# Optimization experiments

Measured on AMD Instinct MI355X. Metric: run time of the kernel, lower is better.

## Reference

```python
import jax, jax.numpy as jnp
import numpy as np

B, T, I, H = 64, 128, 1024, 4096
NNZ_IH, NNZ_HH = 262144, 1048576
LN_EPS = 1e-5


def spmm(rows, cols, vals, x, n_out):
    # y[r, b] = sum_{e: rows[e]==r} vals[e] * x[cols[e], b]
    return jax.ops.segment_sum(vals[:, None] * x[cols], rows, num_segments=n_out)


def setup_inputs() -> dict:
    key = jax.random.key(0)
    ks = jax.random.split(key, 8)
    x = jax.random.normal(ks[0], (B, T, I), dtype=jnp.float32)
    ih_rows = jax.random.randint(ks[1], (NNZ_IH,), 0, H, dtype=jnp.int32)
    ih_cols = jax.random.randint(ks[2], (NNZ_IH,), 0, I, dtype=jnp.int32)
    ih_vals = jax.random.normal(ks[3], (NNZ_IH,), dtype=jnp.float32) * 0.02
    hh_rows = jax.random.randint(ks[4], (NNZ_HH,), 0, H, dtype=jnp.int32)
    hh_cols = jax.random.randint(ks[5], (NNZ_HH,), 0, H, dtype=jnp.int32)
    hh_vals = jax.random.normal(ks[6], (NNZ_HH,), dtype=jnp.float32) * 0.02
    return {
        "x": x,
        "ih_rows": ih_rows, "ih_cols": ih_cols, "ih_vals": ih_vals,
        "hh_rows": hh_rows, "hh_cols": hh_cols, "hh_vals": hh_vals,
        "b_ih": jnp.zeros((H,), jnp.float32),
        "b_hh": jnp.zeros((H,), jnp.float32),
        "ln_gamma": jnp.ones((H,), jnp.float32),
        "ln_beta": jnp.zeros((H,), jnp.float32),
    }


def reference(x, ih_rows, ih_cols, ih_vals, hh_rows, hh_cols, hh_vals,
              b_ih, b_hh, ln_gamma, ln_beta):
    # batch_first input (B, T, I) -> (T, I, B), matching torch permute(1, 2, 0)
    xt = jnp.transpose(x, (1, 2, 0))

    def step(h, x_t):
        pre = (spmm(ih_rows, ih_cols, ih_vals, x_t, H) + b_ih[:, None]
               + spmm(hh_rows, hh_cols, hh_vals, h, H) + b_hh[:, None])
        h_act = jnp.tanh(pre)  # (H, B)
        # layernorm over hidden dim (applied on h.t() in torch)
        mu = jnp.mean(h_act, axis=0, keepdims=True)
        var = jnp.mean((h_act - mu) ** 2, axis=0, keepdims=True)
        h_norm = (h_act - mu) * jax.lax.rsqrt(var + LN_EPS)
        h_new = h_norm * ln_gamma[:, None] + ln_beta[:, None]
        return h_new, h_new

    h0 = jnp.zeros((H, B), jnp.float32)
    h_last, out = jax.lax.scan(step, h0, xt)  # out: (T, H, B)
    out = jnp.transpose(out, (2, 0, 1))       # (B, T, H) batch_first
    h_last = h_last.T                         # (B, H)
    return out, h_last
```

## Files before the change

### kernel.cpp

```cpp
#include <hip/hip_runtime.h>
#include <hip/hip_bf16.h>
#include <cstdint>

#define TT 128
#define BB 64
#define II 1024
#define HD 4096
#define N_IH 262144
#define N_HH 1048576
#define LN_EPS 1e-5f
#define NREP 16

typedef unsigned int u32;
typedef unsigned short u16;
typedef float f32x2 __attribute__((ext_vector_type(2)));

__device__ __forceinline__ u32 f2bf_bits(float f) {
  u32 u = __float_as_uint(f);
  return (u + 0x7FFFu + ((u >> 16) & 1u)) >> 16;
}


__global__ void k_hist(const int* __restrict__ rows, int n, int* __restrict__ hist) {
  int e = blockIdx.x * 256 + threadIdx.x;
  if (e < n) atomicAdd(&hist[rows[e] * 64 + (blockIdx.x & 63)], 1);
}

__global__ __launch_bounds__(256) void k_rowtot(const int* __restrict__ hist, int* __restrict__ rowtot) {
  int w = threadIdx.x >> 6, lane = threadIdx.x & 63;
  int row = blockIdx.x * 4 + w;
  int c = hist[row * 64 + lane];
#pragma unroll
  for (int d = 1; d < 64; d <<= 1) c += __shfl_xor(c, d);
  if (lane == 0) rowtot[row] = (c + 7) & ~7;
}

__global__ void k_scan2(const int* __restrict__ rowtot, int* __restrict__ rp) {
  int lane = threadIdx.x;
  int total = 0;
  for (int j = 0; j < 64; ++j) total += rowtot[lane * 64 + j];
  int x = total;
  for (int d = 1; d < 64; d <<= 1) {
    int y = __shfl_up(x, d, 64);
    if (lane >= d) x += y;
  }
  int run = x - total;
  for (int j = 0; j < 64; ++j) {
    int idx = lane * 64 + j;
    rp[idx] = run;
    run += rowtot[idx];
  }
  if (lane == 63) rp[HD] = run;
}

__global__ __launch_bounds__(256) void k_repbase(const int* __restrict__ hist, const int* __restrict__ rp,
                                                 int* __restrict__ cur) {
  int w = threadIdx.x >> 6, lane = threadIdx.x & 63;
  int row = blockIdx.x * 4 + w;
  int c = hist[row * 64 + lane];
  int x = c;
#pragma unroll
  for (int d = 1; d < 64; d <<= 1) {
    int y = __shfl_up(x, d, 64);
    if (lane >= d) x += y;
  }
  cur[row * 64 + lane] = rp[row] + (x - c);
}

__global__ void k_scatter(const int* __restrict__ rows, const int* __restrict__ cols,
                          const float* __restrict__ vals, int n,
                          int* __restrict__ cur, u32* __restrict__ meta,
                          const float* __restrict__ gamma, const float* __restrict__ beta,
                          float* __restrict__ rvg_rep, float* __restrict__ rvb_rep, int fold) {
  int e = blockIdx.x * 256 + threadIdx.x;
  if (e >= n) return;
  int rep = blockIdx.x & 63;
  int r = rows[e], c = cols[e];
  float v = vals[e];
  float vg = v;
  if (fold) {
    vg = v * gamma[c];
    atomicAdd(&rvg_rep[r * 64 + rep], vg);
    atomicAdd(&rvb_rep[r * 64 + rep], v * beta[c]);
  }
  u32 word = (f2bf_bits(vg) << 16) | (u32)c;
  int pos = atomicAdd(&cur[r * 64 + rep], 1);
  meta[pos] = word;
}

__global__ __launch_bounds__(256) void k_rvred(const float* __restrict__ rvg_rep,
                                               const float* __restrict__ rvb_rep,
                                               float* __restrict__ rowvg, float* __restrict__ rowvb) {
  int w = threadIdx.x >> 6, lane = threadIdx.x & 63;
  int row = blockIdx.x * 4 + w;
  float a = rvg_rep[row * 64 + lane];
  float b = rvb_rep[row * 64 + lane];
#pragma unroll
  for (int d = 1; d < 64; d <<= 1) { a += __shfl_xor(a, d); b += __shfl_xor(b, d); }
  if (lane == 0) { rowvg[row] = a; rowvb[row] = b; }
}

__global__ __launch_bounds__(256) void k_xt(const float* __restrict__ x, u16* __restrict__ xt) {
  __shared__ u16 tile[64][66];
  int t = blockIdx.x >> 4, i0 = (blockIdx.x & 15) << 6;
  int w = threadIdx.x >> 6, lane = threadIdx.x & 63;
#pragma unroll
  for (int k = 0; k < 16; ++k) {
    int b = w * 16 + k;
    float v = x[((size_t)b * TT + t) * II + i0 + lane];
    tile[b][lane] = (u16)f2bf_bits(v);
  }
  __syncthreads();
#pragma unroll
  for (int k = 0; k < 16; ++k) {
    int i = w * 16 + k;
    xt[((size_t)t * II + i0 + i) * BB + lane] = tile[lane][i];
  }
}


__device__ __forceinline__ uint4 gld(const char* base, u32 m) {
  return *(const uint4*)(base + ((int)(m & 0xFFFFu) << 7));
}

__device__ __forceinline__ void consume(u32 m, uint4 g, f32x2 acc[4]) {
  float vgf = __uint_as_float(m & 0xFFFF0000u);
  f32x2 vg2 = {vgf, vgf};
  f32x2 p0 = {__uint_as_float(g.x << 16), __uint_as_float(g.x & 0xFFFF0000u)};
  f32x2 p1 = {__uint_as_float(g.y << 16), __uint_as_float(g.y & 0xFFFF0000u)};
  f32x2 p2 = {__uint_as_float(g.z << 16), __uint_as_float(g.z & 0xFFFF0000u)};
  f32x2 p3 = {__uint_as_float(g.w << 16), __uint_as_float(g.w & 0xFFFF0000u)};
  acc[0] += vg2 * p0;
  acc[1] += vg2 * p1;
  acc[2] += vg2 * p2;
  acc[3] += vg2 * p3;
}

__device__ __forceinline__ void gatherL(const u32* __restrict__ lm, int n,
                                        const char* __restrict__ base, f32x2 acc[4]) {
  if (n <= 0) return;
  u32 m0 = lm[0], m1 = lm[8], m2 = lm[16], m3 = lm[24], m4 = lm[32], m5 = lm[40];
  uint4 g0 = gld(base, m0), g1 = gld(base, m1), g2 = gld(base, m2), g3 = gld(base, m3);
#pragma unroll 4
  for (int it = 0; it < n; ++it) {
    u32 m6 = lm[(it + 6) * 8];
    uint4 g4 = gld(base, m4);
    consume(m0, g0, acc);
    m0 = m1; m1 = m2; m2 = m3; m3 = m4; m4 = m5; m5 = m6;
    g0 = g1; g1 = g2; g2 = g3; g3 = g4;
  }
}

__global__ __launch_bounds__(256, 8) void k_step(
    const u32* __restrict__ meta_ih, const int* __restrict__ rp_ih,
    const u32* __restrict__ meta_hh, const int* __restrict__ rp_hh,
    const u16* __restrict__ xt_t, const u16* __restrict__ Aprev,
    u16* __restrict__ Acur,
    const float* __restrict__ st_prev, float* __restrict__ st_cur,
    const float* __restrict__ b_ih, const float* __restrict__ b_hh,
    const float* __restrict__ rowvg, const float* __restrict__ rowvb, int first) {
  __shared__ float s_mu[64], s_rs[64], s_sum[64], s_sq[64];
  __shared__ float epil[4][2][64];
  __shared__ __align__(16) u32 lmeta_hh[2][768];
  __shared__ __align__(16) u32 lmeta_ih[2][256];
  int tid = threadIdx.x;
  int w = tid >> 6, lane = tid & 63;
  int r0 = blockIdx.x * 2;

  if (w < 2) {
    if (!first) {
      int s0 = rp_hh[r0 + w];
      const uint4* src = (const uint4*)(meta_hh + s0);
      uint4* dst = (uint4*)(&lmeta_hh[w][0]);
#pragma unroll
      for (int k = 0; k < 3; ++k) dst[k * 64 + lane] = src[k * 64 + lane];
    }
  } else if (w == 2) {
#pragma unroll
    for (int i = 0; i < 2; ++i) {
      int s0 = rp_ih[r0 + i];
      ((uint4*)&lmeta_ih[i][0])[lane] = ((const uint4*)(meta_ih + s0))[lane];
    }
  } else {
    s_sum[lane] = 0.f;
    s_sq[lane] = 0.f;
    if (!first) {
      float s = 0.f, q = 0.f;
#pragma unroll
      for (int r2 = 0; r2 < NREP; ++r2) {
        s += st_prev[r2 * 64 + lane];
        q += st_prev[NREP * 64 + r2 * 64 + lane];
      }
      float mu = s * (1.0f / HD);
      float var = q * (1.0f / HD) - mu * mu;
      s_mu[lane] = mu;
      s_rs[lane] = rsqrtf(var + LN_EPS);
    }
  }
  __syncthreads();

  int row = r0 + (w >> 1);
  int half = w & 1;
  int grp = lane >> 3;
  int l = lane & 7;

  f32x2 acc[4] = {{0,0},{0,0},{0,0},{0,0}};
  {
    int n = (rp_ih[row + 1] - rp_ih[row]) >> 3;
    int nA = (n + 1) >> 1;
    int nn = half ? (n - nA) : nA;
    const u32* lm = &lmeta_ih[w >> 1][(half ? nA * 8 : 0) + grp];
    gatherL(lm, nn, (const char*)xt_t + l * 16, acc);
  }
#pragma unroll
  for (int j = 0; j < 4; ++j) {
#pragma unroll
    for (int d = 8; d < 64; d <<= 1) {
      acc[j].x += __shfl_xor(acc[j].x, d);
      acc[j].y += __shfl_xor(acc[j].y, d);
    }
  }
  if (lane < 8) {
#pragma unroll
    for (int j = 0; j < 4; ++j) {
      epil[w][0][lane * 8 + 2 * j] = acc[j].x;
      epil[w][0][lane * 8 + 2 * j + 1] = acc[j].y;
    }
  }

#pragma unroll
  for (int j = 0; j < 4; ++j) { acc[j].x = 0.f; acc[j].y = 0.f; }
  if (!first) {
    int n = (rp_hh[row + 1] - rp_hh[row]) >> 3;
    int nA = (n + 1) >> 1;
    int nn = half ? (n - nA) : nA;
    const u32* lm = &lmeta_hh[w >> 1][(half ? nA * 8 : 0) + grp];
    gatherL(lm, nn, (const char*)Aprev + l * 16, acc);
  }
#pragma unroll
  for (int j = 0; j < 4; ++j) {
#pragma unroll
    for (int d = 8; d < 64; d <<= 1) {
      acc[j].x += __shfl_xor(acc[j].x, d);
      acc[j].y += __shfl_xor(acc[j].y, d);
    }
  }
  if (lane < 8) {
#pragma unroll
    for (int j = 0; j < 4; ++j) {
      epil[w][1][lane * 8 + 2 * j] = acc[j].x;
      epil[w][1][lane * 8 + 2 * j + 1] = acc[j].y;
    }
  }

  __syncthreads();
  if (tid < 128) {
    int ridx = tid >> 6;
    int b = tid & 63;
    int row_e = r0 + ridx;
    float S_ih = epil[ridx * 2][0][b] + epil[ridx * 2 + 1][0][b];
    float bih = b_ih[row_e], bhh = b_hh[row_e];
    float pre;
    if (first) {
      pre = S_ih + bih + bhh;
    } else {
      float S_hh = epil[ridx * 2][1][b] + epil[ridx * 2 + 1][1][b];
      pre = S_ih + s_rs[b] * (S_hh - s_mu[b] * rowvg[row_e]) + (bih + bhh + rowvb[row_e]);
    }
    float h = 1.0f - 2.0f / (__expf(2.0f * pre) + 1.0f);
    Acur[(size_t)row_e * BB + b] = (u16)f2bf_bits(h);
    atomicAdd(&s_sum[b], h);
    atomicAdd(&s_sq[b], h * h);
  }
  __syncthreads();
  if (tid < 64) {
    int rep = blockIdx.x & (NREP - 1);
    atomicAdd(&st_cur[rep * 64 + tid], s_sum[tid]);
    atomicAdd(&st_cur[NREP * 64 + rep * 64 + tid], s_sq[tid]);
  }
}


__global__ __launch_bounds__(256) void k_out(const u16* __restrict__ A,
                                             const float* __restrict__ stats,
                                             const float* __restrict__ gamma,
                                             const float* __restrict__ beta,
                                             float* __restrict__ out) {
  __shared__ float s_mu[64], s_rs[64];
  __shared__ float tile[64][65];
  int t = blockIdx.x >> 6, r0 = (blockIdx.x & 63) << 6;
  int tid = threadIdx.x, w = tid >> 6, lane = tid & 63;
  const float* st = stats + (size_t)t * (2 * NREP * 64);
  if (tid < 64) {
    float s = 0.f, q = 0.f;
#pragma unroll
    for (int r2 = 0; r2 < NREP; ++r2) {
      s += st[r2 * 64 + tid];
      q += st[NREP * 64 + r2 * 64 + tid];
    }
    float mu = s * (1.0f / HD);
    float var = q * (1.0f / HD) - mu * mu;
    s_mu[tid] = mu;
    s_rs[tid] = rsqrtf(var + LN_EPS);
  }
  __syncthreads();
#pragma unroll
  for (int k = 0; k < 16; ++k) {
    int r = r0 + w * 16 + k;
    float a = __uint_as_float(((u32)A[((size_t)t * HD + r) * BB + lane]) << 16);
    float hn = (a - s_mu[lane]) * s_rs[lane] * gamma[r] + beta[r];
    tile[w * 16 + k][lane] = hn;
  }
  __syncthreads();
#pragma unroll
  for (int k = 0; k < 16; ++k) {
    int b = w * 16 + k;
    float v = tile[lane][b];
    out[((size_t)b * TT + t) * HD + r0 + lane] = v;
    if (t == TT - 1) out[(size_t)BB * TT * HD + (size_t)b * HD + r0 + lane] = v;
  }
}


extern "C" void kernel_launch(void* const* d_in, const int* in_sizes, int n_in,
                              void* d_out, int out_size, void* d_ws, size_t ws_size,
                              hipStream_t stream) {
  const float* x = (const float*)d_in[0];
  const int* ih_rows = (const int*)d_in[1];
  const int* ih_cols = (const int*)d_in[2];
  const float* ih_vals = (const float*)d_in[3];
  const int* hh_rows = (const int*)d_in[4];
  const int* hh_cols = (const int*)d_in[5];
  const float* hh_vals = (const float*)d_in[6];
  const float* b_ih = (const float*)d_in[7];
  const float* b_hh = (const float*)d_in[8];
  const float* gamma = (const float*)d_in[9];
  const float* beta = (const float*)d_in[10];

  char* ws = (char*)d_ws;
  u16* xt = (u16*)(ws + 0);
  u16* A = (u16*)(ws + 16777216);
  u32* meta_ih = (u32*)(ws + 83886080);
  u32* meta_hh = (u32*)(ws + 85065984);
  float* stats = (float*)(ws + 89391616);
  float* rowvg = (float*)(ws + 90440192);
  float* rowvb = (float*)(ws + 90456576);
  int* rp_ih = (int*)(ws + 90472960);
  int* rp_hh = (int*)(ws + 90489600);

  char* scr = ws + 50331648;
  int* hist_ih = (int*)(scr + 0);
  int* hist_hh = (int*)(scr + 1048576);
  int* cur_ih = (int*)(scr + 2097152);
  int* cur_hh = (int*)(scr + 3145728);
  float* rvg_rep = (float*)(scr + 4194304);
  float* rvb_rep = (float*)(scr + 5242880);
  int* rowtot_ih = (int*)(scr + 6291456);
  int* rowtot_hh = (int*)(scr + 6307840);

  hipMemsetAsync(scr, 0, 6291456, stream);
  hipMemsetAsync(ws + 83886080, 0, 6554112, stream);

  k_hist<<<N_IH / 256, 256, 0, stream>>>(ih_rows, N_IH, hist_ih);
  k_hist<<<N_HH / 256, 256, 0, stream>>>(hh_rows, N_HH, hist_hh);
  k_rowtot<<<HD / 4, 256, 0, stream>>>(hist_ih, rowtot_ih);
  k_rowtot<<<HD / 4, 256, 0, stream>>>(hist_hh, rowtot_hh);
  k_scan2<<<1, 64, 0, stream>>>(rowtot_ih, rp_ih);
  k_scan2<<<1, 64, 0, stream>>>(rowtot_hh, rp_hh);
  k_repbase<<<HD / 4, 256, 0, stream>>>(hist_ih, rp_ih, cur_ih);
  k_repbase<<<HD / 4, 256, 0, stream>>>(hist_hh, rp_hh, cur_hh);
  k_scatter<<<N_IH / 256, 256, 0, stream>>>(ih_rows, ih_cols, ih_vals, N_IH, cur_ih, meta_ih,
                                            gamma, beta, rvg_rep, rvb_rep, 0);
  k_scatter<<<N_HH / 256, 256, 0, stream>>>(hh_rows, hh_cols, hh_vals, N_HH, cur_hh, meta_hh,
                                            gamma, beta, rvg_rep, rvb_rep, 1);
  k_rvred<<<HD / 4, 256, 0, stream>>>(rvg_rep, rvb_rep, rowvg, rowvb);
  k_xt<<<TT * (II / 64), 256, 0, stream>>>(x, xt);

  for (int t = 0; t < TT; ++t) {
    const u16* xt_t = xt + (size_t)t * II * BB;
    const u16* Aprev = (t == 0) ? A : A + (size_t)(t - 1) * HD * BB;
    u16* Acur = A + (size_t)t * HD * BB;
    const float* st_prev = (t == 0) ? stats : stats + (size_t)(t - 1) * (2 * NREP * 64);
    float* st_cur = stats + (size_t)t * (2 * NREP * 64);
    k_step<<<HD / 2, 256, 0, stream>>>(meta_ih, rp_ih, meta_hh, rp_hh, xt_t, Aprev, Acur,
                                       st_prev, st_cur, b_ih, b_hh, rowvg, rowvb,
                                       (t == 0) ? 1 : 0);
  }

  k_out<<<TT * (HD / 64), 256, 0, stream>>>(A, stats, gamma, beta, (float*)d_out);
}
```

Measured before the change: 2.330 ms.

## Fuse all timesteps into one persistent cooperative kernel with grid barrier

Replaces the 128 per-timestep k_step launches with a single cooperative persistent kernel that loops over time and synchronizes blocks through a two-level atomic tree barrier. Each block also loads its sparse row metadata into LDS once instead of every step. This targets per-launch overhead and the repeated metadata staging, at the cost of spin-wait barrier latency and a requirement that all 2048 blocks be co-resident. A bounded spin that can break out risks silent incorrect ordering, and the old per-step path is kept only as a fallback if the cooperative launch fails.

```diff
diff --git a/kernel.cpp b/kernel.cpp
--- a/kernel.cpp
+++ b/kernel.cpp
@@ -151,6 +151,153 @@
   }
 }
 
+__global__ __launch_bounds__(256, 8) void k_steps(
+    const u32* __restrict__ meta_ih, const int* __restrict__ rp_ih,
+    const u32* __restrict__ meta_hh, const int* __restrict__ rp_hh,
+    const u16* __restrict__ xt, u16* __restrict__ A,
+    float* __restrict__ stats,
+    const float* __restrict__ b_ih, const float* __restrict__ b_hh,
+    const float* __restrict__ rowvg, const float* __restrict__ rowvb,
+    int* __restrict__ bar) {
+  __shared__ float s_mu[64], s_rs[64], s_sum[64], s_sq[64];
+  __shared__ float epil[4][2][64];
+  __shared__ __align__(16) u32 lmeta_hh[2][768];
+  __shared__ __align__(16) u32 lmeta_ih[2][256];
+  int tid = threadIdx.x;
+  int w = tid >> 6, lane = tid & 63;
+  int r0 = blockIdx.x * 2;
+
+  if (w < 2) {
+    int s0 = rp_hh[r0 + w];
+    const uint4* src = (const uint4*)(meta_hh + s0);
+    uint4* dst = (uint4*)(&lmeta_hh[w][0]);
+#pragma unroll
+    for (int k = 0; k < 3; ++k) dst[k * 64 + lane] = src[k * 64 + lane];
+  } else if (w == 2) {
+#pragma unroll
+    for (int i = 0; i < 2; ++i) {
+      int s0 = rp_ih[r0 + i];
+      ((uint4*)&lmeta_ih[i][0])[lane] = ((const uint4*)(meta_ih + s0))[lane];
+    }
+  }
+
+  int row = r0 + (w >> 1);
+  int half = w & 1;
+  int grp = lane >> 3;
+  int l16 = (lane & 7) * 16;
+  int n_ih = (rp_ih[row + 1] - rp_ih[row]) >> 3;
+  int nA_ih = (n_ih + 1) >> 1;
+  int nn_ih = half ? (n_ih - nA_ih) : nA_ih;
+  const u32* lm_ih = &lmeta_ih[w >> 1][(half ? nA_ih * 8 : 0) + grp];
+  int n_hh = (rp_hh[row + 1] - rp_hh[row]) >> 3;
+  int nA_hh = (n_hh + 1) >> 1;
+  int nn_hh = half ? (n_hh - nA_hh) : nA_hh;
+  const u32* lm_hh = &lmeta_hh[w >> 1][(half ? nA_hh * 8 : 0) + grp];
+
+  int row_e = r0 + (tid >> 6);
+  float bsum0 = 0.f, bsum = 0.f, rvg_r = 0.f;
+  if (tid < 128) {
+    float bi = b_ih[row_e], bh = b_hh[row_e];
+    bsum0 = bi + bh;
+    bsum = bi + bh + rowvb[row_e];
+    rvg_r = rowvg[row_e];
+  }
+  int leaf = (int)(blockIdx.x & 63) * 32;
+  __syncthreads();
+
+  for (int t = 0; t < TT; ++t) {
+    if (w == 3) {
+      s_sum[lane] = 0.f;
+      s_sq[lane] = 0.f;
+      if (t > 0) {
+        const float* st_prev = stats + (size_t)(t - 1) * (2 * NREP * 64);
+        float s = 0.f, q = 0.f;
+#pragma unroll
+        for (int r2 = 0; r2 < NREP; ++r2) {
+          s += st_prev[r2 * 64 + lane];
+          q += st_prev[NREP * 64 + r2 * 64 + lane];
+        }
+        float mu = s * (1.0f / HD);
+        float var = q * (1.0f / HD) - mu * mu;
+        s_mu[lane] = mu;
+        s_rs[lane] = rsqrtf(var + LN_EPS);
+      }
+    }
+
+    const char* xb = (const char*)(xt + (size_t)t * II * BB) + l16;
+    f32x2 acc_ih[4] = {{0,0},{0,0},{0,0},{0,0}};
+    gatherL(lm_ih, nn_ih, xb, acc_ih);
+    f32x2 acc_hh[4] = {{0,0},{0,0},{0,0},{0,0}};
+    if (t > 0) {
+      const char* ab = (const char*)(A + (size_t)(t - 1) * HD * BB) + l16;
+      gatherL(lm_hh, nn_hh, ab, acc_hh);
+    }
+#pragma unroll
+    for (int j = 0; j < 4; ++j) {
+#pragma unroll
+      for (int d = 8; d < 64; d <<= 1) {
+        acc_ih[j].x += __shfl_xor(acc_ih[j].x, d);
+        acc_ih[j].y += __shfl_xor(acc_ih[j].y, d);
+        acc_hh[j].x += __shfl_xor(acc_hh[j].x, d);
+        acc_hh[j].y += __shfl_xor(acc_hh[j].y, d);
+      }
+    }
+    if (lane < 8) {
+#pragma unroll
+      for (int j = 0; j < 4; ++j) {
+        epil[w][0][lane * 8 + 2 * j] = acc_ih[j].x;
+        epil[w][0][lane * 8 + 2 * j + 1] = acc_ih[j].y;
+        epil[w][1][lane * 8 + 2 * j] = acc_hh[j].x;
+        epil[w][1][lane * 8 + 2 * j + 1] = acc_hh[j].y;
+      }
+    }
+    __syncthreads();
+
+    if (tid < 128) {
+      int ridx = tid >> 6, b = tid & 63;
+      float S_ih = epil[ridx * 2][0][b] + epil[ridx * 2 + 1][0][b];
+      float pre;
+      if (t == 0) {
+        pre = S_ih + bsum0;
+      } else {
+        float S_hh = epil[ridx * 2][1][b] + epil[ridx * 2 + 1][1][b];
+        pre = S_ih + s_rs[b] * (S_hh - s_mu[b] * rvg_r) + bsum;
+      }
+      float h = 1.0f - 2.0f / (__expf(2.0f * pre) + 1.0f);
+      __hip_atomic_store(&A[(size_t)t * HD * BB + (size_t)row_e * BB + b],
+                         (u16)f2bf_bits(h), __ATOMIC_RELAXED, __HIP_MEMORY_SCOPE_AGENT);
+      atomicAdd(&s_sum[b], h);
+      atomicAdd(&s_sq[b], h * h);
+    }
+    __syncthreads();
+    if (tid < 64) {
+      int rep = blockIdx.x & (NREP - 1);
+      float* st_cur = stats + (size_t)t * (2 * NREP * 64);
+      atomicAdd(&st_cur[rep * 64 + tid], s_sum[tid]);
+      atomicAdd(&st_cur[NREP * 64 + rep * 64 + tid], s_sq[tid]);
+    }
+
+    if (t < TT - 1) {
+      if (tid == 0) {
+        int gen = t + 1;
+        int prev = __hip_atomic_fetch_add(&bar[leaf], 1, __ATOMIC_RELEASE, __HIP_MEMORY_SCOPE_AGENT);
+        if (prev == gen * 32 - 1) {
+          int r = __hip_atomic_fetch_add(&bar[2048], 1, __ATOMIC_ACQ_REL, __HIP_MEMORY_SCOPE_AGENT);
+          if (r == gen * 64 - 1)
+            __hip_atomic_store(&bar[2080], gen, __ATOMIC_RELEASE, __HIP_MEMORY_SCOPE_AGENT);
+        }
+        int spin = 0;
+        while (__hip_atomic_load(&bar[2080], __ATOMIC_RELAXED, __HIP_MEMORY_SCOPE_AGENT) < gen) {
+          if (++spin > (1 << 20)) break;
+        }
+        (void)__hip_atomic_load(&bar[2080], __ATOMIC_ACQUIRE, __HIP_MEMORY_SCOPE_AGENT);
+      }
+      __syncthreads();
+    }
+  }
+}
+
+
 __global__ __launch_bounds__(256, 8) void k_step(
     const u32* __restrict__ meta_ih, const int* __restrict__ rp_ih,
     const u32* __restrict__ meta_hh, const int* __restrict__ rp_hh,
@@ -347,6 +494,7 @@
   float* rowvb = (float*)(ws + 90456576);
   int* rp_ih = (int*)(ws + 90472960);
   int* rp_hh = (int*)(ws + 90489600);
+  int* bar = (int*)(ws + 90506240);
 
   char* scr = ws + 50331648;
   int* hist_ih = (int*)(scr + 0);
@@ -360,6 +508,7 @@
 
   hipMemsetAsync(scr, 0, 6291456, stream);
   hipMemsetAsync(ws + 83886080, 0, 6554112, stream);
+  hipMemsetAsync(ws + 90506240, 0, 8448, stream);
 
   k_hist<<<N_IH / 256, 256, 0, stream>>>(ih_rows, N_IH, hist_ih);
   k_hist<<<N_HH / 256, 256, 0, stream>>>(hh_rows, N_HH, hist_hh);
@@ -376,15 +525,23 @@
   k_rvred<<<HD / 4, 256, 0, stream>>>(rvg_rep, rvb_rep, rowvg, rowvb);
   k_xt<<<TT * (II / 64), 256, 0, stream>>>(x, xt);
 
-  for (int t = 0; t < TT; ++t) {
-    const u16* xt_t = xt + (size_t)t * II * BB;
-    const u16* Aprev = (t == 0) ? A : A + (size_t)(t - 1) * HD * BB;
-    u16* Acur = A + (size_t)t * HD * BB;
-    const float* st_prev = (t == 0) ? stats : stats + (size_t)(t - 1) * (2 * NREP * 64);
-    float* st_cur = stats + (size_t)t * (2 * NREP * 64);
-    k_step<<<HD / 2, 256, 0, stream>>>(meta_ih, rp_ih, meta_hh, rp_hh, xt_t, Aprev, Acur,
-                                       st_prev, st_cur, b_ih, b_hh, rowvg, rowvb,
-                                       (t == 0) ? 1 : 0);
+  void* args[] = {
+      (void*)&meta_ih, (void*)&rp_ih, (void*)&meta_hh, (void*)&rp_hh,
+      (void*)&xt, (void*)&A, (void*)&stats,
+      (void*)&b_ih, (void*)&b_hh, (void*)&rowvg, (void*)&rowvb, (void*)&bar};
+  hipError_t ce = hipLaunchCooperativeKernel((const void*)k_steps, dim3(HD / 2), dim3(256),
+                                             args, 0, stream);
+  if (ce != hipSuccess) {
+    for (int t = 0; t < TT; ++t) {
+      const u16* xt_t = xt + (size_t)t * II * BB;
+      const u16* Aprev = (t == 0) ? A : A + (size_t)(t - 1) * HD * BB;
+      u16* Acur = A + (size_t)t * HD * BB;
+      const float* st_prev = (t == 0) ? stats : stats + (size_t)(t - 1) * (2 * NREP * 64);
+      float* st_cur = stats + (size_t)t * (2 * NREP * 64);
+      k_step<<<HD / 2, 256, 0, stream>>>(meta_ih, rp_ih, meta_hh, rp_hh, xt_t, Aprev, Acur,
+                                         st_prev, st_cur, b_ih, b_hh, rowvg, rowvb,
+                                         (t == 0) ? 1 : 0);
+    }
   }
 
   k_out<<<TT * (HD / 64), 256, 0, stream>>>(A, stats, gamma, beta, (float*)d_out);
```

After: 6.291 ms. 2.7x slower.
